# Kernel optimization log

Measured on AMD Instinct MI355X. Metric: run time of the kernel, lower is better.

Reference implementation:

```python
import jax, jax.numpy as jnp
import numpy as np

N, E, H, K = 2000, 512, 8, 32
DH = E // H  # 64
CLAMP = 10000.0
LN_EPS = 1e-5


def _layernorm(x, g, b):
    mu = jnp.mean(x, axis=-1, keepdims=True)
    var = jnp.mean((x - mu) ** 2, axis=-1, keepdims=True)
    return (x - mu) * jax.lax.rsqrt(var + LN_EPS) * g + b


def setup_inputs() -> dict:
    key = jax.random.key(0)
    ks = jax.random.split(key, 16)
    s_in = 1.0 / np.sqrt(E)
    inp = {
        'x': jax.random.normal(ks[0], (N, E), jnp.float32),
        'coords9': jax.random.normal(ks[1], (N, 9), jnp.float32),
        'prompt_signal': jax.random.normal(ks[2], (E,), jnp.float32),
        # pos_encoder: Linear(3, E//4) + GELU + LayerNorm(E//4)
        'pos_w1': jax.random.normal(ks[3], (E // 4, 3), jnp.float32) * 0.5,
        'pos_b1': jax.random.normal(ks[4], (E // 4,), jnp.float32) * 0.02,
        'pos_ln_g': jnp.ones((E // 4,), jnp.float32),
        'pos_ln_b': jnp.zeros((E // 4,), jnp.float32),
        # MultiheadAttention in/out projections
        'wq': jax.random.normal(ks[5], (E, E), jnp.float32) * s_in,
        'wk': jax.random.normal(ks[6], (E, E), jnp.float32) * s_in,
        'wv': jax.random.normal(ks[7], (E, E), jnp.float32) * s_in,
        'bq': jnp.zeros((E,), jnp.float32),
        'bk': jnp.zeros((E,), jnp.float32),
        'bv': jnp.zeros((E,), jnp.float32),
        'wo': jax.random.normal(ks[8], (E, E), jnp.float32) * s_in,
        'bo': jnp.zeros((E,), jnp.float32),
    }
    return inp


def reference(x, coords9, prompt_signal, pos_w1, pos_b1, pos_ln_g, pos_ln_b,
              wq, wk, wv, bq, bk, bv, wo, bo):
    n = x.shape[0]
    # centroids of triangle faces: (N,3)
    centroids = coords9.reshape(n, 3, 3).mean(axis=1)
    # pairwise centroid distances (only relation feature that affects output)
    diff = centroids[:, None, :] - centroids[None, :, :]        # (N,N,3)
    distances = jnp.linalg.norm(diff, axis=-1)                   # (N,N)
    # positional encoding branch
    pos_enc = _layernorm(jax.nn.gelu(centroids @ pos_w1.T + pos_b1, approximate=False),
                         pos_ln_g, pos_ln_b)                     # (N,E/4)
    prompt_enhanced = x + prompt_signal[None, :]
    pos_enhanced = jnp.concatenate([prompt_enhanced[:, :3 * E // 4], pos_enc], axis=-1)  # (N,E)
    # top-k nearest neighbors mask (k smallest distances per row)
    _, topk_idx = jax.lax.top_k(-distances, K)                   # (N,K)
    attn_mask = jnp.full((n, n), -jnp.inf, jnp.float32)
    attn_mask = attn_mask.at[jnp.arange(n)[:, None], topk_idx].set(0.0)
    # multi-head attention, self q=k=v, fp32
    q = (pos_enhanced @ wq.T + bq).reshape(n, H, DH)
    k = (pos_enhanced @ wk.T + bk).reshape(n, H, DH)
    v = (pos_enhanced @ wv.T + bv).reshape(n, H, DH)
    scores = jnp.einsum('nhd,mhd->hnm', q, k) / np.sqrt(DH) + attn_mask[None]
    attn = jax.nn.softmax(scores, axis=-1)                       # (H,N,N)
    ctx = jnp.einsum('hnm,mhd->nhd', attn, v).reshape(n, E)
    out = ctx @ wo.T + bo
    # _sanitize_tensor
    out = jnp.nan_to_num(out, nan=0.0, posinf=CLAMP, neginf=-CLAMP)
    return jnp.clip(out, -CLAMP, CLAMP)
```

## Files before the change

### kernel.cpp

```cpp
#include <hip/hip_runtime.h>
#include <math.h>

#define NN_K 32
#define E_DIM 512
#define CLAMP_V 10000.0f

typedef __attribute__((ext_vector_type(8))) short short8;
typedef __attribute__((ext_vector_type(4))) float f32x4;

__device__ __forceinline__ unsigned short f2bf(float x) {
  unsigned u = __float_as_uint(x);
  unsigned r = u + 0x7fffu + ((u >> 16) & 1u);
  return (unsigned short)(r >> 16);
}
__device__ __forceinline__ float bf2f_bits(short h) {
  return __uint_as_float(((unsigned)(unsigned short)h) << 16);
}

__device__ __forceinline__ void async16(const void* g, void* l) {
  __builtin_amdgcn_global_load_lds((const __attribute__((address_space(1))) void*)g,
                                   (__attribute__((address_space(3))) void*)l, 16, 0, 0);
}

__global__ __launch_bounds__(256) void front_kernel(
    const float* __restrict__ x, const float* __restrict__ coords9,
    const float* __restrict__ prompt,
    const float* __restrict__ w1, const float* __restrict__ b1,
    const float* __restrict__ ln_g, const float* __restrict__ ln_b,
    const float* __restrict__ wq, const float* __restrict__ wk,
    const float* __restrict__ wv, const float* __restrict__ wo,
    short* __restrict__ w_bf, short* __restrict__ pos_bf,
    float* __restrict__ cent, int N)
{
  int blk = blockIdx.x;
  int t = threadIdx.x;

  if (blk < 256) {
    #pragma unroll
    for (int i = 0; i < 4; ++i) {
      int v = blk * 256 + t + i * 65536;
      int m = v >> 16;
      int e = v & 0xffff;
      const float* src = m == 0 ? wq : (m == 1 ? wk : (m == 2 ? wv : wo));
      float4 f = ((const float4*)src)[e];
      short4 h;
      h.x = (short)f2bf(f.x); h.y = (short)f2bf(f.y);
      h.z = (short)f2bf(f.z); h.w = (short)f2bf(f.w);
      ((short4*)w_bf)[v] = h;
    }
    return;
  }

  int n = blk - 256;
  size_t rb = (size_t)n * E_DIM;
  if (n >= N) {
    #pragma unroll
    for (int j = t; j < E_DIM; j += 256) pos_bf[rb + j] = 0;
    return;
  }
  __shared__ float red[4];
  float g = 0.f;
  if (t < 128) {
    const float* c9 = coords9 + n * 9;
    float c0 = (c9[0] + c9[3] + c9[6]) / 3.0f;
    float c1 = (c9[1] + c9[4] + c9[7]) / 3.0f;
    float c2 = (c9[2] + c9[5] + c9[8]) / 3.0f;
    if (t == 0) {
      float4 c; c.x = c0; c.y = c1; c.z = c2; c.w = 0.f;
      ((float4*)cent)[n] = c;
    }
    float pre = c0 * w1[t*3+0] + c1 * w1[t*3+1] + c2 * w1[t*3+2] + b1[t];
    g = 0.5f * pre * (1.0f + erff(pre * 0.70710678118654752440f));
    float s = g;
    #pragma unroll
    for (int o = 32; o > 0; o >>= 1) s += __shfl_xor(s, o);
    if ((t & 63) == 0) red[t >> 6] = s;
  }
  __syncthreads();
  float mu = (red[0] + red[1]) * (1.0f / 128.0f);
  float d = g - mu;
  if (t < 128) {
    float s2 = d * d;
    #pragma unroll
    for (int o = 32; o > 0; o >>= 1) s2 += __shfl_xor(s2, o);
    if ((t & 63) == 0) red[2 + (t >> 6)] = s2;
  }
  __syncthreads();
  if (t < 128) {
    float var = (red[2] + red[3]) * (1.0f / 128.0f);
    float y = d * rsqrtf(var + 1e-5f) * ln_g[t] + ln_b[t];
    pos_bf[rb + 384 + t] = (short)f2bf(y);
  }
  #pragma unroll
  for (int j = t; j < 384; j += 256)
    pos_bf[rb + j] = (short)f2bf(x[rb + j] + prompt[j]);
}

__device__ __forceinline__ void gemm_core(
    char* smem,
    const short* __restrict__ A, const short* __restrict__ W,
    const float* __restrict__ bias,
    float* __restrict__ outf, short* __restrict__ outb,
    int out_ld, int out_c0,
    int M, int row0, int col0, bool doClamp)
{
  short* sA = (short*)smem;
  short* sB = (short*)(smem + 8192);
  int tid = threadIdx.x;
  int cr = tid >> 2;
  int ck = (tid & 3) << 3;
  const short* gA = A + (size_t)(row0 + cr) * 512 + ck;
  const short* gB = W + (size_t)(col0 + cr) * 512 + ck;
  int lo = tid * 8, loB1 = (tid + 256) * 8;
  const size_t rstep = (size_t)64 * 512;

  int lane = tid & 63, wv_ = tid >> 6;
  int wn = wv_ << 5;
  int lr = lane & 15, lq = lane >> 4;

#define STAGE(t, b) do { \
    async16(gA + (t) * 32,         sA + (b) * 2048 + lo); \
    async16(gB + (t) * 32,         sB + (b) * 4096 + lo); \
    async16(gB + (t) * 32 + rstep, sB + (b) * 4096 + loB1); } while (0)

  STAGE(0, 0);
  STAGE(1, 1);

  f32x4 acc[4][2];
  #pragma unroll
  for (int i = 0; i < 4; ++i)
    #pragma unroll
    for (int j = 0; j < 2; ++j)
      acc[i][j] = (f32x4){0.f, 0.f, 0.f, 0.f};

  #pragma unroll
  for (int it = 0; it < 16; ++it) {
    int cur = it & 1;
    if (it == 15) asm volatile("s_waitcnt vmcnt(0)\ns_barrier" ::: "memory");
    else          asm volatile("s_waitcnt vmcnt(3)\ns_barrier" ::: "memory");

    short8 af[4], bf[2];
    #pragma unroll
    for (int i = 0; i < 4; ++i)
      af[i] = *(const short8*)&sA[cur * 2048 + ((i << 4) + lr) * 32 + (lq << 3)];
    #pragma unroll
    for (int j = 0; j < 2; ++j)
      bf[j] = *(const short8*)&sB[cur * 4096 + (wn + (j << 4) + lr) * 32 + (lq << 3)];
    #pragma unroll
    for (int i = 0; i < 4; ++i)
      #pragma unroll
      for (int j = 0; j < 2; ++j)
        acc[i][j] = __builtin_amdgcn_mfma_f32_16x16x32_bf16(af[i], bf[j], acc[i][j], 0, 0, 0);

    asm volatile("s_waitcnt lgkmcnt(0)\ns_barrier" ::: "memory");
    if (it + 2 < 16) STAGE(it + 2, cur);
  }
#undef STAGE

  #pragma unroll
  for (int j = 0; j < 2; ++j) {
    int gcol = col0 + wn + (j << 4) + lr;
    float bv_ = bias[gcol];
    #pragma unroll
    for (int i = 0; i < 4; ++i) {
      #pragma unroll
      for (int r = 0; r < 4; ++r) {
        int grow = row0 + (i << 4) + (lq << 2) + r;
        if (grow < M) {
          float v = acc[i][j][r] + bv_;
          if (doClamp) {
            v = isnan(v) ? 0.0f : v;
            v = fminf(fmaxf(v, -CLAMP_V), CLAMP_V);
          }
          if (outf) outf[(size_t)grow * 512 + gcol] = v;
          else      outb[(size_t)grow * out_ld + out_c0 + gcol] = (short)f2bf(v);
        }
      }
    }
  }
}

__global__ __launch_bounds__(256) void qkv_topk(
    const short* __restrict__ A, const short* __restrict__ Wb,
    const float* __restrict__ bq, const float* __restrict__ bk, const float* __restrict__ bv,
    float* __restrict__ qb, short* __restrict__ kv,
    const float* __restrict__ cent, int* __restrict__ topk,
    int M, int N)
{
  __shared__ __align__(16) char smem[24576];
  __shared__ unsigned waveSums[4];
  __shared__ unsigned selB, selNeed;
  __shared__ unsigned cnt, tcnt;

  int by = blockIdx.y;
  if (by < 12) {
    int sel = by >> 2;
    int nblk = by & 3;
    int r0 = blockIdx.x * 64, c0 = nblk * 128;
    if (sel == 0)
      gemm_core(smem, A, Wb, bq, qb, nullptr, 512, 0, M, r0, c0, false);
    else if (sel == 1)
      gemm_core(smem, A, Wb + 262144, bk, nullptr, kv, 1024, 0, M, r0, c0, false);
    else
      gemm_core(smem, A, Wb + 2 * 262144, bv, nullptr, kv, 1024, 512, M, r0, c0, false);
    return;
  }

  int n = (by - 12) * gridDim.x + blockIdx.x;
  if (n >= N) return;

  unsigned* wh   = (unsigned*)smem;
  unsigned* tieB = (unsigned*)(smem + 16384);
  unsigned* tieI = (unsigned*)(smem + 20480);

  int t = threadIdx.x;
  int lane = t & 63, wid = t >> 6;
  const float4* cq = (const float4*)cent;
  float4 c = cq[n];
  float cx = c.x, cy = c.y, cz = c.z;

  #pragma unroll
  for (int i = 0; i < 16; ++i) wh[t + i * 256] = 0;

  unsigned bits[8];
  #pragma unroll
  for (int r = 0; r < 8; ++r) {
    int m = t + (r << 8);
    unsigned b = 0xFFFFFFFFu;
    if (m < N) {
      float4 cm = cq[m];
      float dx = cx - cm.x, dy = cy - cm.y, dz = cz - cm.z;
      float dist = sqrtf(dx*dx + dy*dy + dz*dz);
      b = __float_as_uint(dist);
    }
    bits[r] = b;
  }
  __syncthreads();

  unsigned* myh = wh + (wid << 10);
  #pragma unroll
  for (int r = 0; r < 8; ++r) {
    if (bits[r] != 0xFFFFFFFFu) {
      unsigned bin = bits[r] >> 20;
      atomicAdd(&myh[bin >> 1], 1u << ((bin & 1) << 4));
    }
  }
  __syncthreads();

  unsigned bc[8];
  unsigned tot = 0;
  #pragma unroll
  for (int w = 0; w < 4; ++w) {
    int iw = (t << 2) + w;
    unsigned s = wh[iw] + wh[1024 + iw] + wh[2048 + iw] + wh[3072 + iw];
    bc[w * 2]     = s & 0xFFFFu;
    bc[w * 2 + 1] = s >> 16;
    tot += (s & 0xFFFFu) + (s >> 16);
  }
  unsigned scan = tot;
  #pragma unroll
  for (int o = 1; o < 64; o <<= 1) {
    unsigned u = __shfl_up(scan, o);
    if (lane >= o) scan += u;
  }
  if (lane == 63) waveSums[wid] = scan;
  __syncthreads();
  unsigned off = 0;
  for (int w = 0; w < wid; ++w) off += waveSums[w];
  unsigned incl = scan + off;
  unsigned excl = incl - tot;
  if (excl < NN_K && incl >= NN_K) {
    unsigned cacc = excl;
    #pragma unroll
    for (int b = 0; b < 8; ++b) {
      if (cacc + bc[b] >= NN_K) { selB = (unsigned)(t * 8 + b); selNeed = NN_K - cacc; break; }
      cacc += bc[b];
    }
  }
  if (t == 0) { cnt = 0; tcnt = 0; }
  __syncthreads();

  unsigned B = selB;
  #pragma unroll
  for (int r = 0; r < 8; ++r) {
    if (bits[r] != 0xFFFFFFFFu) {
      unsigned bin = bits[r] >> 20;
      if (bin < B) {
        unsigned slot = atomicAdd(&cnt, 1u);
        topk[n * NN_K + slot] = t + (r << 8);
      } else if (bin == B) {
        unsigned tp = atomicAdd(&tcnt, 1u);
        if (tp < 1024u) { tieB[tp] = bits[r]; tieI[tp] = (unsigned)(t + (r << 8)); }
      }
    }
  }
  __syncthreads();

  if (t < 64) {
    unsigned base = cnt;
    unsigned need = selNeed;
    unsigned tn = tcnt > 1024u ? 1024u : tcnt;
    for (unsigned j = lane; j < tn; j += 64) {
      unsigned kb = tieB[j], ki = tieI[j];
      unsigned rank = 0;
      for (unsigned i = 0; i < tn; ++i) {
        unsigned ib = tieB[i];
        rank += (ib < kb) || (ib == kb && tieI[i] < ki);
      }
      if (rank < need) topk[n * NN_K + base + rank] = (int)ki;
    }
  }
}

__global__ __launch_bounds__(256) void out_mfma(
    const short* __restrict__ A, const short* __restrict__ Wb,
    const float* __restrict__ bias, float* __restrict__ out, int M)
{
  __shared__ __align__(16) char smem[24576];
  gemm_core(smem, A, Wb + (size_t)3 * 262144, bias, out, nullptr, 512, 0, M,
            blockIdx.x * 64, blockIdx.y * 128, true);
}

__global__ __launch_bounds__(512) void attn_kernel(
    const float* __restrict__ qb, const short* __restrict__ kv,
    const int* __restrict__ topk, short* __restrict__ ctx_bf, int N)
{
  __shared__ int sidx[NN_K];
  __shared__ float plds[8 * 32];

  int n = blockIdx.x;
  int tid = threadIdx.x;
  size_t rb = (size_t)n * E_DIM;
  if (n >= N) { ctx_bf[rb + tid] = 0; return; }

  if (tid < NN_K) sidx[tid] = topk[n * NN_K + tid];
  __syncthreads();

  int h = tid >> 6, lane = tid & 63;
  int jk = lane & 31, half = lane >> 5;
  int dbase = h * 64 + half * 32;

  float qv[32];
  {
    const float4* qs = (const float4*)(qb + rb + dbase);
    #pragma unroll
    for (int b = 0; b < 8; ++b) {
      float4 f = qs[b];
      qv[b*4+0] = f.x; qv[b*4+1] = f.y; qv[b*4+2] = f.z; qv[b*4+3] = f.w;
    }
  }

  float s = 0.f;
  {
    const short8* krow = (const short8*)(kv + (size_t)sidx[jk] * 1024 + dbase);
    #pragma unroll
    for (int b = 0; b < 4; ++b) {
      short8 kk = krow[b];
      #pragma unroll
      for (int e = 0; e < 8; ++e)
        s += qv[b * 8 + e] * bf2f_bits(kk[e]);
    }
  }
  s += __shfl_xor(s, 32);
  s *= 0.125f;

  float mx = s;
  #pragma unroll
  for (int o = 16; o > 0; o >>= 1) mx = fmaxf(mx, __shfl_xor(mx, o));
  float p = expf(s - mx);
  float l = p;
  #pragma unroll
  for (int o = 16; o > 0; o >>= 1) l += __shfl_xor(l, o);
  p *= (1.0f / l);
  if (half == 0) plds[h * 32 + jk] = p;
  __syncthreads();

  float pv[32];
  #pragma unroll
  for (int b = 0; b < 8; ++b) {
    float4 f = *(const float4*)&plds[h * 32 + b * 4];
    pv[b*4+0] = f.x; pv[b*4+1] = f.y; pv[b*4+2] = f.z; pv[b*4+3] = f.w;
  }

  int off = 512 + h * 64 + lane;
  float acc = 0.f;
  #pragma unroll
  for (int j = 0; j < NN_K; ++j)
    acc += pv[j] * bf2f_bits(kv[(size_t)sidx[j] * 1024 + off]);
  ctx_bf[rb + h * 64 + lane] = (short)f2bf(acc);
}

extern "C" void kernel_launch(void* const* d_in, const int* in_sizes, int n_in,
                              void* d_out, int out_size, void* d_ws, size_t ws_size,
                              hipStream_t stream) {
  const float* x       = (const float*)d_in[0];
  const float* coords9 = (const float*)d_in[1];
  const float* prompt  = (const float*)d_in[2];
  const float* pos_w1  = (const float*)d_in[3];
  const float* pos_b1  = (const float*)d_in[4];
  const float* ln_g    = (const float*)d_in[5];
  const float* ln_b    = (const float*)d_in[6];
  const float* wq      = (const float*)d_in[7];
  const float* wk      = (const float*)d_in[8];
  const float* wv      = (const float*)d_in[9];
  const float* bq      = (const float*)d_in[10];
  const float* bk      = (const float*)d_in[11];
  const float* bv      = (const float*)d_in[12];
  const float* wo      = (const float*)d_in[13];
  const float* bo      = (const float*)d_in[14];

  int N = in_sizes[1] / 9;
  int Mpad = (N + 127) & ~127;
  size_t PE = (size_t)Mpad * E_DIM;

  char* p = (char*)d_ws;
  short* pos_bf = (short*)p; p += PE * 2;
  short* w_bf   = (short*)p; p += (size_t)4 * 512 * 512 * 2;
  float* qb     = (float*)p; p += PE * 4;
  short* kv_bf  = (short*)p; p += PE * 2 * 2;
  short* ctx_bf = (short*)p; p += PE * 2;
  int*   topk   = (int*)p;   p += (size_t)Mpad * NN_K * 4;
  float* cent   = (float*)p;

  front_kernel<<<256 + Mpad, 256, 0, stream>>>(
      x, coords9, prompt, pos_w1, pos_b1, ln_g, ln_b,
      wq, wk, wv, wo, w_bf, pos_bf, cent, N);

  int gx = Mpad / 64;
  dim3 gq(gx, 12 + (N + gx - 1) / gx);
  qkv_topk<<<gq, 256, 0, stream>>>(pos_bf, w_bf, bq, bk, bv, qb, kv_bf,
                                   cent, topk, Mpad, N);
  attn_kernel<<<Mpad, 512, 0, stream>>>(qb, kv_bf, topk, ctx_bf, N);

  dim3 go(Mpad / 64, 4);
  out_mfma<<<go, 256, 0, stream>>>(ctx_bf, w_bf, bo, (float*)d_out, N);
}
```

Before: 140.9 us.

## Fuse all stages into one persistent kernel with grid-wide barriers

```diff
diff --git a/kernel.cpp b/kernel.cpp
--- a/kernel.cpp
+++ b/kernel.cpp
@@ -4,6 +4,7 @@
 #define NN_K 32
 #define E_DIM 512
 #define CLAMP_V 10000.0f
+#define NBLK 512
 
 typedef __attribute__((ext_vector_type(8))) short short8;
 typedef __attribute__((ext_vector_type(4))) float f32x4;
@@ -22,78 +23,23 @@
                                    (__attribute__((address_space(3))) void*)l, 16, 0, 0);
 }
 
-__global__ __launch_bounds__(256) void front_kernel(
-    const float* __restrict__ x, const float* __restrict__ coords9,
-    const float* __restrict__ prompt,
-    const float* __restrict__ w1, const float* __restrict__ b1,
-    const float* __restrict__ ln_g, const float* __restrict__ ln_b,
-    const float* __restrict__ wq, const float* __restrict__ wk,
-    const float* __restrict__ wv, const float* __restrict__ wo,
-    short* __restrict__ w_bf, short* __restrict__ pos_bf,
-    float* __restrict__ cent, int N)
-{
-  int blk = blockIdx.x;
-  int t = threadIdx.x;
-
-  if (blk < 256) {
-    #pragma unroll
-    for (int i = 0; i < 4; ++i) {
-      int v = blk * 256 + t + i * 65536;
-      int m = v >> 16;
-      int e = v & 0xffff;
-      const float* src = m == 0 ? wq : (m == 1 ? wk : (m == 2 ? wv : wo));
-      float4 f = ((const float4*)src)[e];
-      short4 h;
-      h.x = (short)f2bf(f.x); h.y = (short)f2bf(f.y);
-      h.z = (short)f2bf(f.z); h.w = (short)f2bf(f.w);
-      ((short4*)w_bf)[v] = h;
-    }
-    return;
-  }
-
-  int n = blk - 256;
-  size_t rb = (size_t)n * E_DIM;
-  if (n >= N) {
-    #pragma unroll
-    for (int j = t; j < E_DIM; j += 256) pos_bf[rb + j] = 0;
-    return;
-  }
-  __shared__ float red[4];
-  float g = 0.f;
-  if (t < 128) {
-    const float* c9 = coords9 + n * 9;
-    float c0 = (c9[0] + c9[3] + c9[6]) / 3.0f;
-    float c1 = (c9[1] + c9[4] + c9[7]) / 3.0f;
-    float c2 = (c9[2] + c9[5] + c9[8]) / 3.0f;
-    if (t == 0) {
-      float4 c; c.x = c0; c.y = c1; c.z = c2; c.w = 0.f;
-      ((float4*)cent)[n] = c;
-    }
-    float pre = c0 * w1[t*3+0] + c1 * w1[t*3+1] + c2 * w1[t*3+2] + b1[t];
-    g = 0.5f * pre * (1.0f + erff(pre * 0.70710678118654752440f));
-    float s = g;
-    #pragma unroll
-    for (int o = 32; o > 0; o >>= 1) s += __shfl_xor(s, o);
-    if ((t & 63) == 0) red[t >> 6] = s;
-  }
-  __syncthreads();
-  float mu = (red[0] + red[1]) * (1.0f / 128.0f);
-  float d = g - mu;
-  if (t < 128) {
-    float s2 = d * d;
-    #pragma unroll
-    for (int o = 32; o > 0; o >>= 1) s2 += __shfl_xor(s2, o);
-    if ((t & 63) == 0) red[2 + (t >> 6)] = s2;
-  }
-  __syncthreads();
-  if (t < 128) {
-    float var = (red[2] + red[3]) * (1.0f / 128.0f);
-    float y = d * rsqrtf(var + 1e-5f) * ln_g[t] + ln_b[t];
-    pos_bf[rb + 384 + t] = (short)f2bf(y);
-  }
-  #pragma unroll
-  for (int j = t; j < 384; j += 256)
-    pos_bf[rb + j] = (short)f2bf(x[rb + j] + prompt[j]);
+__device__ __forceinline__ void grid_bar(unsigned* bar, int idx, int nb) {
+  __syncthreads();
+  __threadfence();
+  if (threadIdx.x == 0) {
+    atomicAdd(&bar[idx], 1u);
+    unsigned spin = 0;
+    while (atomicAdd(&bar[idx], 0u) < (unsigned)nb) {
+      __builtin_amdgcn_s_sleep(2);
+      if (++spin > (1u << 20)) break;
+    }
+  }
+  __syncthreads();
+  __threadfence();
+}
+
+__global__ __launch_bounds__(64) void init_bar(unsigned* bar) {
+  if (threadIdx.x < 8) bar[threadIdx.x] = 0;
 }
 
 __device__ __forceinline__ void gemm_core(
@@ -180,35 +126,11 @@
   }
 }
 
-__global__ __launch_bounds__(256) void qkv_topk(
-    const short* __restrict__ A, const short* __restrict__ Wb,
-    const float* __restrict__ bq, const float* __restrict__ bk, const float* __restrict__ bv,
-    float* __restrict__ qb, short* __restrict__ kv,
-    const float* __restrict__ cent, int* __restrict__ topk,
-    int M, int N)
+__device__ __forceinline__ void topk_unit(
+    int n, const float* __restrict__ cent, int* __restrict__ topk, int N,
+    char* smem, unsigned* waveSums, unsigned& selB, unsigned& selNeed,
+    unsigned& cnt, unsigned& tcnt)
 {
-  __shared__ __align__(16) char smem[24576];
-  __shared__ unsigned waveSums[4];
-  __shared__ unsigned selB, selNeed;
-  __shared__ unsigned cnt, tcnt;
-
-  int by = blockIdx.y;
-  if (by < 12) {
-    int sel = by >> 2;
-    int nblk = by & 3;
-    int r0 = blockIdx.x * 64, c0 = nblk * 128;
-    if (sel == 0)
-      gemm_core(smem, A, Wb, bq, qb, nullptr, 512, 0, M, r0, c0, false);
-    else if (sel == 1)
-      gemm_core(smem, A, Wb + 262144, bk, nullptr, kv, 1024, 0, M, r0, c0, false);
-    else
-      gemm_core(smem, A, Wb + 2 * 262144, bv, nullptr, kv, 1024, 512, M, r0, c0, false);
-    return;
-  }
-
-  int n = (by - 12) * gridDim.x + blockIdx.x;
-  if (n >= N) return;
-
   unsigned* wh   = (unsigned*)smem;
   unsigned* tieB = (unsigned*)(smem + 16384);
   unsigned* tieI = (unsigned*)(smem + 20480);
@@ -312,82 +234,198 @@
   }
 }
 
-__global__ __launch_bounds__(256) void out_mfma(
-    const short* __restrict__ A, const short* __restrict__ Wb,
-    const float* __restrict__ bias, float* __restrict__ out, int M)
+__device__ __forceinline__ void attn_row(
+    int n, const float* __restrict__ qb, const short* __restrict__ kv,
+    const int* __restrict__ topk, short* __restrict__ ctx_bf, char* smem, int N)
+{
+  int* sidx = (int*)smem;
+  float* plds = (float*)(smem + 128);
+  int tid = threadIdx.x;
+  size_t rb = (size_t)n * E_DIM;
+
+  if (n >= N) {
+    #pragma unroll
+    for (int j = tid; j < E_DIM; j += 256) ctx_bf[rb + j] = 0;
+    return;
+  }
+
+  if (tid < NN_K) sidx[tid] = topk[n * NN_K + tid];
+  __syncthreads();
+
+  int h4 = tid >> 6, lane = tid & 63;
+  int jk = lane & 31, half = lane >> 5;
+
+  #pragma unroll
+  for (int hi = 0; hi < 2; ++hi) {
+    int hh = h4 + hi * 4;
+    int dbase = hh * 64 + half * 32;
+
+    float qv[32];
+    {
+      const float4* qs = (const float4*)(qb + rb + dbase);
+      #pragma unroll
+      for (int b = 0; b < 8; ++b) {
+        float4 f = qs[b];
+        qv[b*4+0] = f.x; qv[b*4+1] = f.y; qv[b*4+2] = f.z; qv[b*4+3] = f.w;
+      }
+    }
+
+    float s = 0.f;
+    {
+      const short8* krow = (const short8*)(kv + (size_t)sidx[jk] * 1024 + dbase);
+      #pragma unroll
+      for (int b = 0; b < 4; ++b) {
+        short8 kk = krow[b];
+        #pragma unroll
+        for (int e = 0; e < 8; ++e)
+          s += qv[b * 8 + e] * bf2f_bits(kk[e]);
+      }
+    }
+    s += __shfl_xor(s, 32);
+    s *= 0.125f;
+
+    float mx = s;
+    #pragma unroll
+    for (int o = 16; o > 0; o >>= 1) mx = fmaxf(mx, __shfl_xor(mx, o));
+    float p = expf(s - mx);
+    float l = p;
+    #pragma unroll
+    for (int o = 16; o > 0; o >>= 1) l += __shfl_xor(l, o);
+    p *= (1.0f / l);
+    if (half == 0) plds[hh * 32 + jk] = p;
+    __syncthreads();
+
+    float pv[32];
+    #pragma unroll
+    for (int b = 0; b < 8; ++b) {
+      float4 f = *(const float4*)&plds[hh * 32 + b * 4];
+      pv[b*4+0] = f.x; pv[b*4+1] = f.y; pv[b*4+2] = f.z; pv[b*4+3] = f.w;
+    }
+
+    int off = 512 + hh * 64 + lane;
+    float acc = 0.f;
+    #pragma unroll
+    for (int j = 0; j < NN_K; ++j)
+      acc += pv[j] * bf2f_bits(kv[(size_t)sidx[j] * 1024 + off]);
+    ctx_bf[rb + hh * 64 + lane] = (short)f2bf(acc);
+  }
+}
+
+__global__ __launch_bounds__(256, 2) void mega_kernel(
+    const float* __restrict__ x, const float* __restrict__ coords9,
+    const float* __restrict__ prompt,
+    const float* __restrict__ w1, const float* __restrict__ b1,
+    const float* __restrict__ ln_g, const float* __restrict__ ln_b,
+    const float* __restrict__ wq, const float* __restrict__ wk,
+    const float* __restrict__ wv,
+    const float* __restrict__ bq, const float* __restrict__ bk,
+    const float* __restrict__ bv,
+    const float* __restrict__ wo, const float* __restrict__ bo,
+    short* __restrict__ w_bf, short* __restrict__ pos_bf,
+    float* __restrict__ cent, int* __restrict__ topk,
+    float* __restrict__ qb, short* __restrict__ kv,
+    short* __restrict__ ctx_bf, float* __restrict__ outp,
+    unsigned* __restrict__ bar, int N, int Mpad)
 {
   __shared__ __align__(16) char smem[24576];
-  gemm_core(smem, A, Wb + (size_t)3 * 262144, bias, out, nullptr, 512, 0, M,
-            blockIdx.x * 64, blockIdx.y * 128, true);
-}
-
-__global__ __launch_bounds__(512) void attn_kernel(
-    const float* __restrict__ qb, const short* __restrict__ kv,
-    const int* __restrict__ topk, short* __restrict__ ctx_bf, int N)
-{
-  __shared__ int sidx[NN_K];
-  __shared__ float plds[8 * 32];
-
-  int n = blockIdx.x;
-  int tid = threadIdx.x;
-  size_t rb = (size_t)n * E_DIM;
-  if (n >= N) { ctx_bf[rb + tid] = 0; return; }
-
-  if (tid < NN_K) sidx[tid] = topk[n * NN_K + tid];
-  __syncthreads();
-
-  int h = tid >> 6, lane = tid & 63;
-  int jk = lane & 31, half = lane >> 5;
-  int dbase = h * 64 + half * 32;
-
-  float qv[32];
-  {
-    const float4* qs = (const float4*)(qb + rb + dbase);
-    #pragma unroll
-    for (int b = 0; b < 8; ++b) {
-      float4 f = qs[b];
-      qv[b*4+0] = f.x; qv[b*4+1] = f.y; qv[b*4+2] = f.z; qv[b*4+3] = f.w;
-    }
-  }
-
-  float s = 0.f;
-  {
-    const short8* krow = (const short8*)(kv + (size_t)sidx[jk] * 1024 + dbase);
-    #pragma unroll
-    for (int b = 0; b < 4; ++b) {
-      short8 kk = krow[b];
+  __shared__ float red[4];
+  __shared__ unsigned waveSums[4];
+  __shared__ unsigned selB, selNeed, cnt, tcnt;
+
+  int t = threadIdx.x;
+  int nb = gridDim.x;
+
+  for (int u = blockIdx.x; u < 256 + Mpad; u += nb) {
+    if (u < 256) {
       #pragma unroll
-      for (int e = 0; e < 8; ++e)
-        s += qv[b * 8 + e] * bf2f_bits(kk[e]);
-    }
-  }
-  s += __shfl_xor(s, 32);
-  s *= 0.125f;
-
-  float mx = s;
-  #pragma unroll
-  for (int o = 16; o > 0; o >>= 1) mx = fmaxf(mx, __shfl_xor(mx, o));
-  float p = expf(s - mx);
-  float l = p;
-  #pragma unroll
-  for (int o = 16; o > 0; o >>= 1) l += __shfl_xor(l, o);
-  p *= (1.0f / l);
-  if (half == 0) plds[h * 32 + jk] = p;
-  __syncthreads();
-
-  float pv[32];
-  #pragma unroll
-  for (int b = 0; b < 8; ++b) {
-    float4 f = *(const float4*)&plds[h * 32 + b * 4];
-    pv[b*4+0] = f.x; pv[b*4+1] = f.y; pv[b*4+2] = f.z; pv[b*4+3] = f.w;
-  }
-
-  int off = 512 + h * 64 + lane;
-  float acc = 0.f;
-  #pragma unroll
-  for (int j = 0; j < NN_K; ++j)
-    acc += pv[j] * bf2f_bits(kv[(size_t)sidx[j] * 1024 + off]);
-  ctx_bf[rb + h * 64 + lane] = (short)f2bf(acc);
+      for (int i = 0; i < 4; ++i) {
+        int v = u * 256 + t + i * 65536;
+        int m = v >> 16;
+        int e = v & 0xffff;
+        const float* src = m == 0 ? wq : (m == 1 ? wk : (m == 2 ? wv : wo));
+        float4 f = ((const float4*)src)[e];
+        short4 h;
+        h.x = (short)f2bf(f.x); h.y = (short)f2bf(f.y);
+        h.z = (short)f2bf(f.z); h.w = (short)f2bf(f.w);
+        ((short4*)w_bf)[v] = h;
+      }
+    } else {
+      int n = u - 256;
+      size_t rb = (size_t)n * E_DIM;
+      if (n >= N) {
+        #pragma unroll
+        for (int j = t; j < E_DIM; j += 256) pos_bf[rb + j] = 0;
+      } else {
+        float g = 0.f;
+        if (t < 128) {
+          const float* c9 = coords9 + n * 9;
+          float c0 = (c9[0] + c9[3] + c9[6]) / 3.0f;
+          float c1 = (c9[1] + c9[4] + c9[7]) / 3.0f;
+          float c2 = (c9[2] + c9[5] + c9[8]) / 3.0f;
+          if (t == 0) {
+            float4 c; c.x = c0; c.y = c1; c.z = c2; c.w = 0.f;
+            ((float4*)cent)[n] = c;
+          }
+          float pre = c0 * w1[t*3+0] + c1 * w1[t*3+1] + c2 * w1[t*3+2] + b1[t];
+          g = 0.5f * pre * (1.0f + erff(pre * 0.70710678118654752440f));
+          float s = g;
+          #pragma unroll
+          for (int o = 32; o > 0; o >>= 1) s += __shfl_xor(s, o);
+          if ((t & 63) == 0) red[t >> 6] = s;
+        }
+        __syncthreads();
+        float mu = (red[0] + red[1]) * (1.0f / 128.0f);
+        float d = g - mu;
+        if (t < 128) {
+          float s2 = d * d;
+          #pragma unroll
+          for (int o = 32; o > 0; o >>= 1) s2 += __shfl_xor(s2, o);
+          if ((t & 63) == 0) red[2 + (t >> 6)] = s2;
+        }
+        __syncthreads();
+        if (t < 128) {
+          float var = (red[2] + red[3]) * (1.0f / 128.0f);
+          float y = d * rsqrtf(var + 1e-5f) * ln_g[t] + ln_b[t];
+          pos_bf[rb + 384 + t] = (short)f2bf(y);
+        }
+        #pragma unroll
+        for (int j = t; j < 384; j += 256)
+          pos_bf[rb + j] = (short)f2bf(x[rb + j] + prompt[j]);
+      }
+    }
+    __syncthreads();
+  }
+  grid_bar(bar, 0, nb);
+
+  for (int u = blockIdx.x; u < 384 + N; u += nb) {
+    if (u < 384) {
+      int bx = u & 31, by = u >> 5;
+      int sel = by >> 2, nblk = by & 3;
+      int r0 = bx * 64, c0 = nblk * 128;
+      if (sel == 0)
+        gemm_core(smem, pos_bf, w_bf, bq, qb, nullptr, 512, 0, Mpad, r0, c0, false);
+      else if (sel == 1)
+        gemm_core(smem, pos_bf, w_bf + 262144, bk, nullptr, kv, 1024, 0, Mpad, r0, c0, false);
+      else
+        gemm_core(smem, pos_bf, w_bf + 2 * 262144, bv, nullptr, kv, 1024, 512, Mpad, r0, c0, false);
+    } else {
+      topk_unit(u - 384, cent, topk, N, smem, waveSums, selB, selNeed, cnt, tcnt);
+    }
+    __syncthreads();
+  }
+  grid_bar(bar, 1, nb);
+
+  for (int n = blockIdx.x; n < Mpad; n += nb) {
+    attn_row(n, qb, kv, topk, ctx_bf, smem, N);
+    __syncthreads();
+  }
+  grid_bar(bar, 2, nb);
+
+  for (int u = blockIdx.x; u < 128; u += nb) {
+    int bx = u & 31, by = u >> 5;
+    gemm_core(smem, ctx_bf, w_bf + (size_t)3 * 262144, bo, outp, nullptr, 512, 0, N,
+              bx * 64, by * 128, true);
+  }
 }
 
 extern "C" void kernel_launch(void* const* d_in, const int* in_sizes, int n_in,
@@ -420,18 +458,15 @@
   short* kv_bf  = (short*)p; p += PE * 2 * 2;
   short* ctx_bf = (short*)p; p += PE * 2;
   int*   topk   = (int*)p;   p += (size_t)Mpad * NN_K * 4;
-  float* cent   = (float*)p;
-
-  front_kernel<<<256 + Mpad, 256, 0, stream>>>(
+  float* cent   = (float*)p; p += (size_t)Mpad * 16;
+  unsigned* bar = (unsigned*)p;
+
+  float* outp = (float*)d_out;
+
+  init_bar<<<1, 64, 0, stream>>>(bar);
+  mega_kernel<<<NBLK, 256, 0, stream>>>(
       x, coords9, prompt, pos_w1, pos_b1, ln_g, ln_b,
-      wq, wk, wv, wo, w_bf, pos_bf, cent, N);
-
-  int gx = Mpad / 64;
-  dim3 gq(gx, 12 + (N + gx - 1) / gx);
-  qkv_topk<<<gq, 256, 0, stream>>>(pos_bf, w_bf, bq, bk, bv, qb, kv_bf,
-                                   cent, topk, Mpad, N);
-  attn_kernel<<<Mpad, 512, 0, stream>>>(qb, kv_bf, topk, ctx_bf, N);
-
-  dim3 go(Mpad / 64, 4);
-  out_mfma<<<go, 256, 0, stream>>>(ctx_bf, w_bf, bo, (float*)d_out, N);
-}
+      wq, wk, wv, bq, bk, bv, wo, bo,
+      w_bf, pos_bf, cent, topk, qb, kv_bf, ctx_bf, outp,
+      bar, N, Mpad);
+}
```

Result: slower. 449.5 us (+219.0%).
